# Kernel tuning notes

Measured on AMD Instinct MI355X. Metric: run time of the kernel, lower is better.

The kernel has to match this reference:

```python
import jax, jax.numpy as jnp
import numpy as np

N, CIN, COUT, E, NDIR = 65536, 128, 128, 589824, 9


def sel_conv(x, src, dst, sel, W, b):
    # x: [N, Cin]; W: [D, Cin, Cout]; edges j->i: out[i] += x[j] @ W[sel]
    n = x.shape[0]
    xs = x[src]  # [E, Cin] gather
    out = jnp.zeros((n, W.shape[2]), x.dtype)
    for d in range(W.shape[0]):  # fixed small direction count (9 or 1)
        m = (sel == d).astype(x.dtype)[:, None]
        agg = jax.ops.segment_sum(xs * m, dst, num_segments=n)  # [N, Cin]
        out = out + agg @ W[d]
    return out + b


def bn_eval(x, g, be, rm, rv, eps=1e-5):
    return (x - rm) * (g * jax.lax.rsqrt(rv + eps)) + be


def setup_inputs() -> dict:
    key = jax.random.key(0)
    ks = jax.random.split(key, 24)
    s = 0.05
    inp = {
        "x": jax.random.normal(ks[0], (N, CIN), jnp.float32),
        "edge_index": jax.random.randint(ks[1], (2, E), 0, N),
        "selections": jax.random.randint(ks[2], (E,), 0, NDIR),
        "W1": jax.random.normal(ks[3], (NDIR, CIN, COUT), jnp.float32) * s,
        "b1": jax.random.normal(ks[4], (COUT,), jnp.float32) * s,
        "g1": 1.0 + jax.random.normal(ks[5], (COUT,), jnp.float32) * s,
        "be1": jax.random.normal(ks[6], (COUT,), jnp.float32) * s,
        "rm1": jax.random.normal(ks[7], (COUT,), jnp.float32) * s,
        "rv1": 0.5 + jax.random.uniform(ks[8], (COUT,), jnp.float32),
        "W2": jax.random.normal(ks[9], (NDIR, COUT, COUT), jnp.float32) * s,
        "b2": jax.random.normal(ks[10], (COUT,), jnp.float32) * s,
        "g2": 1.0 + jax.random.normal(ks[11], (COUT,), jnp.float32) * s,
        "be2": jax.random.normal(ks[12], (COUT,), jnp.float32) * s,
        "rm2": jax.random.normal(ks[13], (COUT,), jnp.float32) * s,
        "rv2": 0.5 + jax.random.uniform(ks[14], (COUT,), jnp.float32),
        "W3": jax.random.normal(ks[15], (1, CIN, COUT), jnp.float32) * s,
        "b3": jax.random.normal(ks[16], (COUT,), jnp.float32) * s,
        "g3": 1.0 + jax.random.normal(ks[17], (COUT,), jnp.float32) * s,
        "be3": jax.random.normal(ks[18], (COUT,), jnp.float32) * s,
        "rm3": jax.random.normal(ks[19], (COUT,), jnp.float32) * s,
        "rv3": 0.5 + jax.random.uniform(ks[20], (COUT,), jnp.float32),
    }
    return inp


def reference(x, edge_index, selections, W1, b1, g1, be1, rm1, rv1,
              W2, b2, g2, be2, rm2, rv2, W3, b3, g3, be3, rm3, rv3):
    src, dst = edge_index[0], edge_index[1]
    # conv1: SelectionConv(3x3) + BN + ELU
    h = jax.nn.elu(bn_eval(sel_conv(x, src, dst, selections, W1, b1), g1, be1, rm1, rv1))
    # conv2: SelectionConv(3x3) + BN + ELU
    h = jax.nn.elu(bn_eval(sel_conv(h, src, dst, selections, W2, b2), g2, be2, rm2, rv2))
    # conv3: SelectionConv(1x1) shortcut (only selection-0 edges)
    sc = sel_conv(x, src, dst, selections, W3, b3)
    return jax.nn.elu(bn_eval(h + sc, g3, be3, rm3, rv3))
```

## Files before the change

kernel.cpp:

```cpp
#include <hip/hip_runtime.h>
#include <hip/hip_bf16.h>
#include <math.h>

#define N_NODES 65536
#define NDIR 9
#define NEDGE 589824
#define TILE_M 32
#define SLOTS 24
#define OCAP 65536
#define APITCH 136

typedef __attribute__((ext_vector_type(8))) short short8;
typedef __attribute__((ext_vector_type(4))) float f32x4;

__device__ inline float bf2f(unsigned short u){ return __uint_as_float(((unsigned int)u)<<16); }
__device__ inline unsigned short f2bf(float f){
  unsigned int x = __float_as_uint(f);
  x += 0x7fff + ((x>>16)&1);
  return (unsigned short)(x>>16);
}
__device__ inline float elu1(float x){ return x>0.f ? x : expm1f(x); }

__device__ inline void acc8(f32x4& a0, f32x4& a1, short8 v){
  a0[0] += bf2f((unsigned short)v[0]); a0[1] += bf2f((unsigned short)v[1]);
  a0[2] += bf2f((unsigned short)v[2]); a0[3] += bf2f((unsigned short)v[3]);
  a1[0] += bf2f((unsigned short)v[4]); a1[1] += bf2f((unsigned short)v[5]);
  a1[2] += bf2f((unsigned short)v[6]); a1[3] += bf2f((unsigned short)v[7]);
}

__global__ void prep_all(const float* __restrict__ x, unsigned short* __restrict__ xb,
                         const float* __restrict__ W1, const float* __restrict__ W2,
                         const float* __restrict__ W3,
                         const float* __restrict__ b1, const float* __restrict__ g1,
                         const float* __restrict__ be1, const float* __restrict__ rm1,
                         const float* __restrict__ rv1,
                         const float* __restrict__ b2, const float* __restrict__ g2,
                         const float* __restrict__ be2, const float* __restrict__ rm2,
                         const float* __restrict__ rv2,
                         const float* __restrict__ b3, const float* __restrict__ g3,
                         const float* __restrict__ be3, const float* __restrict__ rm3,
                         const float* __restrict__ rv3,
                         unsigned short* __restrict__ Wt1, unsigned short* __restrict__ Wt2,
                         float* __restrict__ bias1, float* __restrict__ bias2,
                         float* __restrict__ bias3, float* __restrict__ s3v,
                         int* __restrict__ cnt, int* __restrict__ ocnt){
  const float eps = 1e-5f;
  int b = blockIdx.x, tid = threadIdx.x;
  if (b < 64){
    int4 z = {0,0,0,0};
    *(int4*)&cnt[(b*256 + tid)*4] = z;
  } else if (b < 1280){
    int idx = (b - 64)*256 + tid;
    if (idx < 1280*128) {
      int n = idx >> 7, k = idx & 127;
      float v;
      if (n < 1152) { int d = n >> 7, c = n & 127;
        float s = g1[c]*rsqrtf(rv1[c]+eps); v = W1[(d*128 + k)*128 + c] * s; }
      else { int c = n - 1152;
        float s = g3[c]*rsqrtf(rv3[c]+eps); v = W3[k*128 + c] * s; }
      Wt1[idx] = f2bf(v);
    } else {
      int j = idx - 1280*128;
      int n = j >> 7, k = j & 127;
      int d = n >> 7, c = n & 127;
      float s = g2[c]*rsqrtf(rv2[c]+eps);
      Wt2[j] = f2bf(W2[(d*128 + k)*128 + c] * s);
    }
  } else if (b == 1280){
    if (tid < 128){
      int c = tid;
      float s1 = g1[c]*rsqrtf(rv1[c]+eps);
      bias1[c] = (b1[c]-rm1[c])*s1 + be1[c];
      float s2 = g2[c]*rsqrtf(rv2[c]+eps);
      bias2[c] = (b2[c]-rm2[c])*s2 + be2[c];
      float s3 = g3[c]*rsqrtf(rv3[c]+eps);
      bias3[c] = (b3[c]-rm3[c])*s3 + be3[c];
      s3v[c] = s3;
    } else if (tid == 128){
      *ocnt = 0;
    }
  } else {
    int i = ((b - 1281)*256 + tid)*8;
    f32x4 f0 = *(const f32x4*)(x + i);
    f32x4 f1 = *(const f32x4*)(x + i + 4);
    short8 t;
    #pragma unroll
    for (int j = 0; j < 4; j++){ t[j] = (short)f2bf(f0[j]); t[4+j] = (short)f2bf(f1[j]); }
    *(short8*)(xb + i) = t;
  }
}

__global__ void scatter_k(const int* __restrict__ src, const int* __restrict__ dst,
                          const int* __restrict__ sel,
                          int* __restrict__ cnt, int* __restrict__ sorted,
                          int* __restrict__ ocnt, int* __restrict__ overflow){
  int e = blockIdx.x*256 + threadIdx.x;
  int d = dst[e];
  int key = src[e] | (sel[e] << 16);
  int pos = atomicAdd(&cnt[d], 1);
  if (pos < SLOTS){
    sorted[d*SLOTS + pos] = key;
  } else {
    int oi = atomicAdd(ocnt, 1);
    if (oi < OCAP){ overflow[oi*2] = d; overflow[oi*2 + 1] = key; }
  }
}

__device__ __forceinline__ void mfma_tile(f32x4 acc[2][2],
                                          const unsigned short* agg,
                                          const unsigned short* __restrict__ Wd,
                                          int w, int q, int r){
  #pragma unroll
  for (int kk = 0; kk < 4; kk++){
    const unsigned short* wp = Wd + (size_t)(w*32 + r)*128 + kk*32 + q*8;
    short8 b0 = *(const short8*)wp;
    short8 b1 = *(const short8*)(wp + 16*128);
    #pragma unroll
    for (int mt = 0; mt < 2; mt++){
      short8 av = *(const short8*)&agg[(mt*16 + r)*APITCH + kk*32 + q*8];
      acc[mt][0] = __builtin_amdgcn_mfma_f32_16x16x32_bf16(av, b0, acc[mt][0], 0, 0, 0);
      acc[mt][1] = __builtin_amdgcn_mfma_f32_16x16x32_bf16(av, b1, acc[mt][1], 0, 0, 0);
    }
  }
}

template<int IS_L2>
__global__ __launch_bounds__(256, 8) void layer_k(
    const unsigned short* __restrict__ H,
    const unsigned short* __restrict__ X,
    const unsigned short* __restrict__ Wf,
    const unsigned short* __restrict__ W3f,
    const int* __restrict__ cntg, const int* __restrict__ sorted,
    const int* __restrict__ ocnt, const int* __restrict__ overflow,
    const float* __restrict__ biasA, const float* __restrict__ bias3,
    const float* __restrict__ s3v,
    unsigned short* __restrict__ outB, float* __restrict__ outF){
  __shared__ __align__(16) unsigned short agg[TILE_M*APITCH];
  __shared__ int skey[TILE_M*SLOTS];
  __shared__ unsigned short skey2[TILE_M*SLOTS];
  __shared__ int cnts[TILE_M];
  __shared__ int po[TILE_M*9];
  __shared__ int wo[TILE_M*9];
  __shared__ int ocs;
  const int tid = threadIdx.x;
  const int w = tid >> 6, lane = tid & 63;
  const int q = lane >> 4, r = lane & 15;
  const int rid = tid >> 4, c = tid & 15;
  const int m0 = blockIdx.x * TILE_M;

  if (tid < TILE_M){ int v = cntg[m0 + tid]; cnts[tid] = v < SLOTS ? v : SLOTS; }
  if (tid == 255){ int v = *ocnt; ocs = v < OCAP ? v : OCAP; }
  for (int i = tid; i < TILE_M*9; i += 256) wo[i] = 0;
  __syncthreads();

  {
    const int nl8 = tid >> 3, sub = tid & 7;
    int e8 = cnts[nl8];
    for (int j = sub; j < e8; j += 8){
      int k = sorted[(m0 + nl8)*SLOTS + j];
      skey[nl8*SLOTS + j] = k;
      atomicAdd(&wo[nl8*9 + (k >> 16)], 1);
    }
  }
  __syncthreads();
  if (tid < TILE_M){
    int base = tid*SLOTS;
    #pragma unroll
    for (int d = 0; d < 9; d++){
      int b = tid*9 + d;
      po[b] = base;
      int cc = wo[b];
      wo[b] = base;
      base += cc;
    }
  }
  __syncthreads();
  {
    const int nl8 = tid >> 3, sub = tid & 7;
    int e8 = cnts[nl8];
    for (int j = sub; j < e8; j += 8){
      int k = skey[nl8*SLOTS + j];
      int pos = atomicAdd(&wo[nl8*9 + (k >> 16)], 1);
      skey2[pos] = (unsigned short)k;
    }
  }
  __syncthreads();

  f32x4 acc[2][2];
  #pragma unroll
  for (int mt = 0; mt < 2; mt++){ acc[mt][0] = (f32x4){0,0,0,0}; acc[mt][1] = (f32x4){0,0,0,0}; }

  #pragma unroll 1
  for (int d = 0; d < 9; d++){
    if (d) __syncthreads();
    {
      int b = rid*9 + d;
      int s = po[b], e = wo[b];
      f32x4 a0 = {0,0,0,0}, a1 = {0,0,0,0};
      for (int i = s; i < e; i++){
        int key = skey2[i];
        short8 v = *(const short8*)(H + (size_t)key*128 + c*8);
        acc8(a0, a1, v);
      }
      for (int i = 0; i < ocs; i++){
        if (overflow[i*2] == m0 + rid && (overflow[i*2+1] >> 16) == d){
          short8 v = *(const short8*)(H + (size_t)(overflow[i*2+1] & 0xFFFF)*128 + c*8);
          acc8(a0, a1, v);
        }
      }
      short8 o;
      o[0]=(short)f2bf(a0[0]); o[1]=(short)f2bf(a0[1]); o[2]=(short)f2bf(a0[2]); o[3]=(short)f2bf(a0[3]);
      o[4]=(short)f2bf(a1[0]); o[5]=(short)f2bf(a1[1]); o[6]=(short)f2bf(a1[2]); o[7]=(short)f2bf(a1[3]);
      *(short8*)&agg[rid*APITCH + c*8] = o;
    }
    {
      int b = (16 + rid)*9 + d;
      int s = po[b], e = wo[b];
      f32x4 a0 = {0,0,0,0}, a1 = {0,0,0,0};
      for (int i = s; i < e; i++){
        int key = skey2[i];
        short8 v = *(const short8*)(H + (size_t)key*128 + c*8);
        acc8(a0, a1, v);
      }
      for (int i = 0; i < ocs; i++){
        if (overflow[i*2] == m0 + 16 + rid && (overflow[i*2+1] >> 16) == d){
          short8 v = *(const short8*)(H + (size_t)(overflow[i*2+1] & 0xFFFF)*128 + c*8);
          acc8(a0, a1, v);
        }
      }
      short8 o;
      o[0]=(short)f2bf(a0[0]); o[1]=(short)f2bf(a0[1]); o[2]=(short)f2bf(a0[2]); o[3]=(short)f2bf(a0[3]);
      o[4]=(short)f2bf(a1[0]); o[5]=(short)f2bf(a1[1]); o[6]=(short)f2bf(a1[2]); o[7]=(short)f2bf(a1[3]);
      *(short8*)&agg[(16 + rid)*APITCH + c*8] = o;
    }
    __syncthreads();
    mfma_tile(acc, agg, Wf + (size_t)d*128*128, w, q, r);
  }

  if constexpr (!IS_L2){
    #pragma unroll
    for (int mt = 0; mt < 2; mt++)
      #pragma unroll
      for (int n2 = 0; n2 < 2; n2++){
        int col = w*32 + n2*16 + r;
        float bA = biasA[col];
        #pragma unroll
        for (int rr = 0; rr < 4; rr++){
          int row = m0 + mt*16 + q*4 + rr;
          outB[(size_t)row*128 + col] = f2bf(elu1(acc[mt][n2][rr] + bA));
        }
      }
  } else {
    __syncthreads();
    #pragma unroll
    for (int t2 = 0; t2 < 2; t2++){
      int nl = t2*16 + rid;
      int b = nl*9;
      int s = po[b], e = wo[b];
      f32x4 a0 = {0,0,0,0}, a1 = {0,0,0,0};
      for (int i = s; i < e; i++){
        int key = skey2[i];
        short8 v = *(const short8*)(X + (size_t)key*128 + c*8);
        acc8(a0, a1, v);
      }
      for (int i = 0; i < ocs; i++){
        if (overflow[i*2] == m0 + nl && (overflow[i*2+1] >> 16) == 0){
          short8 v = *(const short8*)(X + (size_t)(overflow[i*2+1] & 0xFFFF)*128 + c*8);
          acc8(a0, a1, v);
        }
      }
      short8 o;
      o[0]=(short)f2bf(a0[0]); o[1]=(short)f2bf(a0[1]); o[2]=(short)f2bf(a0[2]); o[3]=(short)f2bf(a0[3]);
      o[4]=(short)f2bf(a1[0]); o[5]=(short)f2bf(a1[1]); o[6]=(short)f2bf(a1[2]); o[7]=(short)f2bf(a1[3]);
      *(short8*)&agg[nl*APITCH + c*8] = o;
    }
    __syncthreads();
    f32x4 sca[2][2];
    #pragma unroll
    for (int mt = 0; mt < 2; mt++){ sca[mt][0] = (f32x4){0,0,0,0}; sca[mt][1] = (f32x4){0,0,0,0}; }
    mfma_tile(sca, agg, W3f, w, q, r);
    #pragma unroll
    for (int mt = 0; mt < 2; mt++)
      #pragma unroll
      for (int n2 = 0; n2 < 2; n2++){
        int col = w*32 + n2*16 + r;
        float bA = biasA[col], b3 = bias3[col], s3 = s3v[col];
        #pragma unroll
        for (int rr = 0; rr < 4; rr++){
          int row = m0 + mt*16 + q*4 + rr;
          float h = elu1(acc[mt][n2][rr] + bA);
          outF[(size_t)row*128 + col] = elu1(h*s3 + sca[mt][n2][rr] + b3);
        }
      }
  }
}

extern "C" void kernel_launch(void* const* d_in, const int* in_sizes, int n_in,
                              void* d_out, int out_size, void* d_ws, size_t ws_size,
                              hipStream_t stream){
  const float* x   = (const float*)d_in[0];
  const int*   ei  = (const int*)d_in[1];
  const int*   sel = (const int*)d_in[2];
  const float* W1  = (const float*)d_in[3];
  const float* b1  = (const float*)d_in[4];
  const float* g1  = (const float*)d_in[5];
  const float* be1 = (const float*)d_in[6];
  const float* rm1 = (const float*)d_in[7];
  const float* rv1 = (const float*)d_in[8];
  const float* W2  = (const float*)d_in[9];
  const float* b2  = (const float*)d_in[10];
  const float* g2  = (const float*)d_in[11];
  const float* be2 = (const float*)d_in[12];
  const float* rm2 = (const float*)d_in[13];
  const float* rv2 = (const float*)d_in[14];
  const float* W3  = (const float*)d_in[15];
  const float* b3  = (const float*)d_in[16];
  const float* g3  = (const float*)d_in[17];
  const float* be3 = (const float*)d_in[18];
  const float* rm3 = (const float*)d_in[19];
  const float* rv3 = (const float*)d_in[20];

  char* ws = (char*)d_ws;
  unsigned short* xb   = (unsigned short*)(ws);
  unsigned short* h1   = (unsigned short*)(ws + 16777216);
  unsigned short* Wt1  = (unsigned short*)(ws + 33554432);
  unsigned short* Wt2  = (unsigned short*)(ws + 33882112);
  float* bias1  = (float*)(ws + 34177024);
  float* bias2  = bias1 + 128;
  float* bias3  = bias1 + 256;
  float* s3v    = bias1 + 384;
  int* cnt      = (int*)(ws + 34179072);
  int* ocnt     = (int*)(ws + 34441216);
  int* overflow = (int*)(ws + 34441472);
  int* sorted   = (int*)(ws + 34965760);

  const int* srcp = ei;
  const int* dstp = ei + NEDGE;

  prep_all<<<5377, 256, 0, stream>>>(x, xb, W1, W2, W3,
                                     b1, g1, be1, rm1, rv1,
                                     b2, g2, be2, rm2, rv2,
                                     b3, g3, be3, rm3, rv3,
                                     Wt1, Wt2, bias1, bias2, bias3, s3v,
                                     cnt, ocnt);
  scatter_k<<<NEDGE/256, 256, 0, stream>>>(srcp, dstp, sel, cnt, sorted, ocnt, overflow);

  layer_k<0><<<2048, 256, 0, stream>>>(xb, nullptr, Wt1, nullptr, cnt, sorted,
                                       ocnt, overflow,
                                       bias1, nullptr, nullptr, h1, nullptr);
  layer_k<1><<<2048, 256, 0, stream>>>(h1, xb, Wt2, Wt1 + 1152*128, cnt, sorted,
                                       ocnt, overflow,
                                       bias2, bias3, s3v, nullptr, (float*)d_out);
}
```

Before: 332.5 us.

## Fuse scatter into prep kernel and reuse layer-1 direction-0 aggregate for shortcut

Merges the edge scatter into the prep kernel and replaces the in-kernel zeroing of the counters with a hipMemsetAsync, so one kernel launch goes away. Layer 1 also writes its direction-0 aggregate of x to a workspace buffer. Layer 2 then loads that buffer for the 1x1 shortcut instead of gathering x over selection-0 edges again. This trades a second gather for an extra 16MB write and read. The cached path only runs when the workspace is large enough, which is not known from the code shown.

```diff
diff --git a/kernel.cpp b/kernel.cpp
--- a/kernel.cpp
+++ b/kernel.cpp
@@ -28,29 +28,40 @@
   a1[2] += bf2f((unsigned short)v[6]); a1[3] += bf2f((unsigned short)v[7]);
 }
 
-__global__ void prep_all(const float* __restrict__ x, unsigned short* __restrict__ xb,
-                         const float* __restrict__ W1, const float* __restrict__ W2,
-                         const float* __restrict__ W3,
-                         const float* __restrict__ b1, const float* __restrict__ g1,
-                         const float* __restrict__ be1, const float* __restrict__ rm1,
-                         const float* __restrict__ rv1,
-                         const float* __restrict__ b2, const float* __restrict__ g2,
-                         const float* __restrict__ be2, const float* __restrict__ rm2,
-                         const float* __restrict__ rv2,
-                         const float* __restrict__ b3, const float* __restrict__ g3,
-                         const float* __restrict__ be3, const float* __restrict__ rm3,
-                         const float* __restrict__ rv3,
-                         unsigned short* __restrict__ Wt1, unsigned short* __restrict__ Wt2,
-                         float* __restrict__ bias1, float* __restrict__ bias2,
-                         float* __restrict__ bias3, float* __restrict__ s3v,
-                         int* __restrict__ cnt, int* __restrict__ ocnt){
+__global__ void fuse_k(const float* __restrict__ x, unsigned short* __restrict__ xb,
+                       const float* __restrict__ W1, const float* __restrict__ W2,
+                       const float* __restrict__ W3,
+                       const float* __restrict__ b1, const float* __restrict__ g1,
+                       const float* __restrict__ be1, const float* __restrict__ rm1,
+                       const float* __restrict__ rv1,
+                       const float* __restrict__ b2, const float* __restrict__ g2,
+                       const float* __restrict__ be2, const float* __restrict__ rm2,
+                       const float* __restrict__ rv2,
+                       const float* __restrict__ b3, const float* __restrict__ g3,
+                       const float* __restrict__ be3, const float* __restrict__ rm3,
+                       const float* __restrict__ rv3,
+                       unsigned short* __restrict__ Wt1, unsigned short* __restrict__ Wt2,
+                       float* __restrict__ bias1, float* __restrict__ bias2,
+                       float* __restrict__ bias3, float* __restrict__ s3v,
+                       int* __restrict__ cnt, int* __restrict__ ocnt,
+                       int* __restrict__ overflow,
+                       const int* __restrict__ src, const int* __restrict__ dst,
+                       const int* __restrict__ sel, int* __restrict__ sorted){
   const float eps = 1e-5f;
   int b = blockIdx.x, tid = threadIdx.x;
-  if (b < 64){
-    int4 z = {0,0,0,0};
-    *(int4*)&cnt[(b*256 + tid)*4] = z;
-  } else if (b < 1280){
-    int idx = (b - 64)*256 + tid;
+  if (b < 2304){
+    int e = b*256 + tid;
+    int d = dst[e];
+    int key = src[e] | (sel[e] << 16);
+    int pos = atomicAdd(&cnt[d], 1);
+    if (pos < SLOTS){
+      sorted[d*SLOTS + pos] = key;
+    } else {
+      int oi = atomicAdd(ocnt, 1);
+      if (oi < OCAP){ overflow[oi*2] = d; overflow[oi*2 + 1] = key; }
+    }
+  } else if (b < 3520){
+    int idx = (b - 2304)*256 + tid;
     if (idx < 1280*128) {
       int n = idx >> 7, k = idx & 127;
       float v;
@@ -66,7 +77,7 @@
       float s = g2[c]*rsqrtf(rv2[c]+eps);
       Wt2[j] = f2bf(W2[(d*128 + k)*128 + c] * s);
     }
-  } else if (b == 1280){
+  } else if (b == 3520){
     if (tid < 128){
       int c = tid;
       float s1 = g1[c]*rsqrtf(rv1[c]+eps);
@@ -76,33 +87,15 @@
       float s3 = g3[c]*rsqrtf(rv3[c]+eps);
       bias3[c] = (b3[c]-rm3[c])*s3 + be3[c];
       s3v[c] = s3;
-    } else if (tid == 128){
-      *ocnt = 0;
     }
   } else {
-    int i = ((b - 1281)*256 + tid)*8;
+    int i = ((b - 3521)*256 + tid)*8;
     f32x4 f0 = *(const f32x4*)(x + i);
     f32x4 f1 = *(const f32x4*)(x + i + 4);
     short8 t;
     #pragma unroll
     for (int j = 0; j < 4; j++){ t[j] = (short)f2bf(f0[j]); t[4+j] = (short)f2bf(f1[j]); }
     *(short8*)(xb + i) = t;
-  }
-}
-
-__global__ void scatter_k(const int* __restrict__ src, const int* __restrict__ dst,
-                          const int* __restrict__ sel,
-                          int* __restrict__ cnt, int* __restrict__ sorted,
-                          int* __restrict__ ocnt, int* __restrict__ overflow){
-  int e = blockIdx.x*256 + threadIdx.x;
-  int d = dst[e];
-  int key = src[e] | (sel[e] << 16);
-  int pos = atomicAdd(&cnt[d], 1);
-  if (pos < SLOTS){
-    sorted[d*SLOTS + pos] = key;
-  } else {
-    int oi = atomicAdd(ocnt, 1);
-    if (oi < OCAP){ overflow[oi*2] = d; overflow[oi*2 + 1] = key; }
   }
 }
 
@@ -124,7 +117,7 @@
   }
 }
 
-template<int IS_L2>
+template<int IS_L2, int AGG0>
 __global__ __launch_bounds__(256, 8) void layer_k(
     const unsigned short* __restrict__ H,
     const unsigned short* __restrict__ X,
@@ -134,6 +127,7 @@
     const int* __restrict__ ocnt, const int* __restrict__ overflow,
     const float* __restrict__ biasA, const float* __restrict__ bias3,
     const float* __restrict__ s3v,
+    const unsigned short* __restrict__ agg0r, unsigned short* __restrict__ agg0w,
     unsigned short* __restrict__ outB, float* __restrict__ outF){
   __shared__ __align__(16) unsigned short agg[TILE_M*APITCH];
   __shared__ int skey[TILE_M*SLOTS];
@@ -212,6 +206,8 @@
       o[0]=(short)f2bf(a0[0]); o[1]=(short)f2bf(a0[1]); o[2]=(short)f2bf(a0[2]); o[3]=(short)f2bf(a0[3]);
       o[4]=(short)f2bf(a1[0]); o[5]=(short)f2bf(a1[1]); o[6]=(short)f2bf(a1[2]); o[7]=(short)f2bf(a1[3]);
       *(short8*)&agg[rid*APITCH + c*8] = o;
+      if (AGG0 && !IS_L2 && d == 0)
+        *(short8*)(agg0w + (size_t)(m0 + rid)*128 + c*8) = o;
     }
     {
       int b = (16 + rid)*9 + d;
@@ -232,6 +228,8 @@
       o[0]=(short)f2bf(a0[0]); o[1]=(short)f2bf(a0[1]); o[2]=(short)f2bf(a0[2]); o[3]=(short)f2bf(a0[3]);
       o[4]=(short)f2bf(a1[0]); o[5]=(short)f2bf(a1[1]); o[6]=(short)f2bf(a1[2]); o[7]=(short)f2bf(a1[3]);
       *(short8*)&agg[(16 + rid)*APITCH + c*8] = o;
+      if (AGG0 && !IS_L2 && d == 0)
+        *(short8*)(agg0w + (size_t)(m0 + 16 + rid)*128 + c*8) = o;
     }
     __syncthreads();
     mfma_tile(acc, agg, Wf + (size_t)d*128*128, w, q, r);
@@ -252,27 +250,34 @@
       }
   } else {
     __syncthreads();
-    #pragma unroll
-    for (int t2 = 0; t2 < 2; t2++){
-      int nl = t2*16 + rid;
-      int b = nl*9;
-      int s = po[b], e = wo[b];
-      f32x4 a0 = {0,0,0,0}, a1 = {0,0,0,0};
-      for (int i = s; i < e; i++){
-        int key = skey2[i];
-        short8 v = *(const short8*)(X + (size_t)key*128 + c*8);
-        acc8(a0, a1, v);
-      }
-      for (int i = 0; i < ocs; i++){
-        if (overflow[i*2] == m0 + nl && (overflow[i*2+1] >> 16) == 0){
-          short8 v = *(const short8*)(X + (size_t)(overflow[i*2+1] & 0xFFFF)*128 + c*8);
+    if constexpr (AGG0){
+      short8 vA = *(const short8*)(agg0r + (size_t)(m0 + rid)*128 + c*8);
+      *(short8*)&agg[rid*APITCH + c*8] = vA;
+      short8 vB = *(const short8*)(agg0r + (size_t)(m0 + 16 + rid)*128 + c*8);
+      *(short8*)&agg[(16 + rid)*APITCH + c*8] = vB;
+    } else {
+      #pragma unroll
+      for (int t2 = 0; t2 < 2; t2++){
+        int nl = t2*16 + rid;
+        int b = nl*9;
+        int s = po[b], e = wo[b];
+        f32x4 a0 = {0,0,0,0}, a1 = {0,0,0,0};
+        for (int i = s; i < e; i++){
+          int key = skey2[i];
+          short8 v = *(const short8*)(X + (size_t)key*128 + c*8);
           acc8(a0, a1, v);
         }
-      }
-      short8 o;
-      o[0]=(short)f2bf(a0[0]); o[1]=(short)f2bf(a0[1]); o[2]=(short)f2bf(a0[2]); o[3]=(short)f2bf(a0[3]);
-      o[4]=(short)f2bf(a1[0]); o[5]=(short)f2bf(a1[1]); o[6]=(short)f2bf(a1[2]); o[7]=(short)f2bf(a1[3]);
-      *(short8*)&agg[nl*APITCH + c*8] = o;
+        for (int i = 0; i < ocs; i++){
+          if (overflow[i*2] == m0 + nl && (overflow[i*2+1] >> 16) == 0){
+            short8 v = *(const short8*)(X + (size_t)(overflow[i*2+1] & 0xFFFF)*128 + c*8);
+            acc8(a0, a1, v);
+          }
+        }
+        short8 o;
+        o[0]=(short)f2bf(a0[0]); o[1]=(short)f2bf(a0[1]); o[2]=(short)f2bf(a0[2]); o[3]=(short)f2bf(a0[3]);
+        o[4]=(short)f2bf(a1[0]); o[5]=(short)f2bf(a1[1]); o[6]=(short)f2bf(a1[2]); o[7]=(short)f2bf(a1[3]);
+        *(short8*)&agg[nl*APITCH + c*8] = o;
+      }
     }
     __syncthreads();
     f32x4 sca[2][2];
@@ -333,22 +338,39 @@
   int* ocnt     = (int*)(ws + 34441216);
   int* overflow = (int*)(ws + 34441472);
   int* sorted   = (int*)(ws + 34965760);
+  unsigned short* agg0 = (unsigned short*)(ws + 41257216);
+  const size_t NEED_AGG0 = 41257216ull + 16777216ull;
 
   const int* srcp = ei;
   const int* dstp = ei + NEDGE;
-
-  prep_all<<<5377, 256, 0, stream>>>(x, xb, W1, W2, W3,
-                                     b1, g1, be1, rm1, rv1,
-                                     b2, g2, be2, rm2, rv2,
-                                     b3, g3, be3, rm3, rv3,
-                                     Wt1, Wt2, bias1, bias2, bias3, s3v,
-                                     cnt, ocnt);
-  scatter_k<<<NEDGE/256, 256, 0, stream>>>(srcp, dstp, sel, cnt, sorted, ocnt, overflow);
-
-  layer_k<0><<<2048, 256, 0, stream>>>(xb, nullptr, Wt1, nullptr, cnt, sorted,
-                                       ocnt, overflow,
-                                       bias1, nullptr, nullptr, h1, nullptr);
-  layer_k<1><<<2048, 256, 0, stream>>>(h1, xb, Wt2, Wt1 + 1152*128, cnt, sorted,
-                                       ocnt, overflow,
-                                       bias2, bias3, s3v, nullptr, (float*)d_out);
-}
+  const bool use_agg0 = ws_size >= NEED_AGG0;
+
+  hipMemsetAsync(cnt, 0, 262400, stream);
+  fuse_k<<<7617, 256, 0, stream>>>(x, xb, W1, W2, W3,
+                                   b1, g1, be1, rm1, rv1,
+                                   b2, g2, be2, rm2, rv2,
+                                   b3, g3, be3, rm3, rv3,
+                                   Wt1, Wt2, bias1, bias2, bias3, s3v,
+                                   cnt, ocnt, overflow,
+                                   srcp, dstp, sel, sorted);
+
+  if (use_agg0){
+    layer_k<0,1><<<2048, 256, 0, stream>>>(xb, nullptr, Wt1, nullptr, cnt, sorted,
+                                           ocnt, overflow,
+                                           bias1, nullptr, nullptr,
+                                           nullptr, agg0, h1, nullptr);
+    layer_k<1,1><<<2048, 256, 0, stream>>>(h1, xb, Wt2, Wt1 + 1152*128, cnt, sorted,
+                                           ocnt, overflow,
+                                           bias2, bias3, s3v,
+                                           agg0, nullptr, nullptr, (float*)d_out);
+  } else {
+    layer_k<0,0><<<2048, 256, 0, stream>>>(xb, nullptr, Wt1, nullptr, cnt, sorted,
+                                           ocnt, overflow,
+                                           bias1, nullptr, nullptr,
+                                           nullptr, nullptr, h1, nullptr);
+    layer_k<1,0><<<2048, 256, 0, stream>>>(h1, xb, Wt2, Wt1 + 1152*128, cnt, sorted,
+                                           ocnt, overflow,
+                                           bias2, bias3, s3v,
+                                           nullptr, nullptr, nullptr, (float*)d_out);
+  }
+}
```

Measured after the change: 332.3 us. About the same (-0.1%).
